# Kernel optimization log

Measured on AMD Instinct MI355X. Metric: run time of the kernel, lower is better.

## Reference

```python
import jax, jax.numpy as jnp
import numpy as np

B, T, C = 4, 2048, 1024
H = 16
D = C // H  # head_dim = 64


def setup_inputs() -> dict:
    key = jax.random.key(0)
    ks = jax.random.split(key, 9)
    s = 1.0 / np.sqrt(C)
    return {
        "x": jax.random.normal(ks[0], (B, T, C), dtype=jnp.float32),
        "wq": jax.random.uniform(ks[1], (C, C), jnp.float32, -s, s),
        "bq": jax.random.uniform(ks[2], (C,), jnp.float32, -s, s),
        "wk": jax.random.uniform(ks[3], (C, C), jnp.float32, -s, s),
        "bk": jax.random.uniform(ks[4], (C,), jnp.float32, -s, s),
        "wv": jax.random.uniform(ks[5], (C, C), jnp.float32, -s, s),
        "bv": jax.random.uniform(ks[6], (C,), jnp.float32, -s, s),
        "wo": jax.random.uniform(ks[7], (C, C), jnp.float32, -s, s),
        "bo": jax.random.uniform(ks[8], (C,), jnp.float32, -s, s),
    }


def reference(x, wq, bq, wk, bk, wv, bv, wo, bo):
    # Linear layers (torch convention: y = x @ W.T + b)
    q = x @ wq.T + bq  # [B,T,C]
    k = x @ wk.T + bk
    v = x @ wv.T + bv
    # split heads -> [B,H,T,D]
    q = q.reshape(B, T, H, D).transpose(0, 2, 1, 3)
    k = k.reshape(B, T, H, D).transpose(0, 2, 1, 3)
    v = v.reshape(B, T, H, D).transpose(0, 2, 1, 3)
    scores = jnp.einsum('bhqd,bhkd->bhqk', q, k) / jnp.sqrt(jnp.float32(D))
    causal = jnp.tril(jnp.ones((T, T), dtype=bool))  # position i attends to j<=i
    scores = jnp.where(causal, scores, -jnp.inf)
    attn = jax.nn.softmax(scores, axis=-1)
    # dropout p=0.0 (eval / identity)
    out = jnp.einsum('bhqk,bhkd->bhqd', attn, v)  # [B,H,T,D]
    out = out.transpose(0, 2, 1, 3).reshape(B, T, C)
    return out @ wo.T + bo
```

## Files before the change

### kernel.cpp

```cpp
#include <hip/hip_runtime.h>
#include <stdint.h>

#define B_DIM 4
#define T_DIM 2048
#define C_DIM 1024
#define H_DIM 16
#define D_DIM 64
#define M_DIM (B_DIM * T_DIM)
#define QK_SCALE 0.18033688011112042f

typedef float f32x4 __attribute__((ext_vector_type(4)));
typedef float f32x16 __attribute__((ext_vector_type(16)));
typedef short bf16x8 __attribute__((ext_vector_type(8)));
typedef unsigned short u16;
typedef u16 u16x8 __attribute__((ext_vector_type(8)));

static __device__ __forceinline__ u16 f2b(float f) {
  uint32_t r;
  asm("v_cvt_pk_bf16_f32 %0, %1, %1" : "=v"(r) : "v"(f));
  return (u16)r;
}
static __device__ __forceinline__ uint32_t f2b2(float a, float b) {
  uint32_t r;
  asm("v_cvt_pk_bf16_f32 %0, %1, %2" : "=v"(r) : "v"(a), "v"(b));
  return r;
}

static __device__ __forceinline__ void gl_lds16(const u16* g, u16* l) {
  __builtin_amdgcn_global_load_lds(
      (const __attribute__((address_space(1))) void*)g,
      (__attribute__((address_space(3))) void*)l, 16, 0, 0);
}

__global__ void k_cvt(const float* __restrict__ src, u16* __restrict__ dst, int n4) {
  int i = blockIdx.x * blockDim.x + threadIdx.x;
  if (i < n4) {
    float4 v = ((const float4*)src)[i];
    uint2 o;
    o.x = f2b2(v.x, v.y);
    o.y = f2b2(v.z, v.w);
    ((uint2*)dst)[i] = o;
  }
}

__global__ void k_cvtw(const float* __restrict__ s0, const float* __restrict__ s1,
                       const float* __restrict__ s2, const float* __restrict__ s3,
                       u16* __restrict__ d0, u16* __restrict__ d1,
                       u16* __restrict__ d2, u16* __restrict__ d3) {
  int i = blockIdx.x * blockDim.x + threadIdx.x;
  int seg = i >> 18;
  int j = i & ((1 << 18) - 1);
  const float* s = seg == 0 ? s0 : seg == 1 ? s1 : seg == 2 ? s2 : s3;
  u16* d = seg == 0 ? d0 : seg == 1 ? d1 : seg == 2 ? d2 : d3;
  float4 v = ((const float4*)s)[j];
  uint2 o;
  o.x = f2b2(v.x, v.y);
  o.y = f2b2(v.z, v.w);
  ((uint2*)d)[j] = o;
}

#define NT 16
__global__ __launch_bounds__(512, 2) void k_gemm_qkv(
    const u16* __restrict__ A,
    const u16* __restrict__ w0, const u16* __restrict__ w1, const u16* __restrict__ w2,
    const float* __restrict__ b0, const float* __restrict__ b1, const float* __restrict__ b2,
    u16* __restrict__ Qo, u16* __restrict__ Ko, u16* __restrict__ Vo) {
  __shared__ u16 LA[2][2][256 * 32];
  __shared__ u16 LB[2][2][256 * 32];
  const int tid = threadIdx.x;
  const int l = tid & 63;
  const int w = tid >> 6;
  const int wm = w >> 2, wn = w & 3;
  const int lrow = l & 15, lk = l >> 4;
  const int K = C_DIM;

  const int bid = blockIdx.x;
  const int swz = (bid & 7) * 48 + (bid >> 3);
  const int rowblk = swz / 12, colblk = swz % 12;
  const int seg = colblk >> 2;
  const int brow = rowblk * 256, bcol = (colblk & 3) * 256;

  const u16* Bw = seg == 0 ? w0 : seg == 1 ? w1 : w2;
  const float* bias = seg == 0 ? b0 : seg == 1 ? b1 : b2;
  u16* Out = seg == 0 ? Qo : seg == 1 ? Ko : Vo;
  const float scale = seg == 0 ? QK_SCALE : 1.f;

  const int sr0 = tid >> 2, sc0 = (tid & 3) * 8;
  const int sr1 = (tid + 512) >> 2;

#define STA(db, kh, t)                                                              \
  {                                                                                 \
    gl_lds16(A + (size_t)(brow + sr0) * K + (t) * 64 + (kh) * 32 + sc0,             \
             &LA[db][kh][sr0 * 32 + sc0]);                                          \
    gl_lds16(A + (size_t)(brow + sr1) * K + (t) * 64 + (kh) * 32 + sc0,             \
             &LA[db][kh][sr1 * 32 + sc0]);                                          \
  }
#define STB(db, kh, t)                                                              \
  {                                                                                 \
    gl_lds16(Bw + (size_t)(bcol + sr0) * K + (t) * 64 + (kh) * 32 + sc0,            \
             &LB[db][kh][sr0 * 32 + sc0]);                                          \
    gl_lds16(Bw + (size_t)(bcol + sr1) * K + (t) * 64 + (kh) * 32 + sc0,            \
             &LB[db][kh][sr1 * 32 + sc0]);                                          \
  }
#define LDA_(f, kh, db) (*(const bf16x8*)(&LA[db][kh][(wm * 128 + (f) * 16 + lrow) * 32 + lk * 8]))
#define LDB_(g, kh, db) (*(const bf16x8*)(&LB[db][kh][(wn * 64 + (g) * 16 + lrow) * 32 + lk * 8]))

  f32x4 acc[8][4];
#pragma unroll
  for (int f = 0; f < 8; ++f)
#pragma unroll
    for (int g = 0; g < 4; ++g) acc[f][g] = (f32x4){0.f, 0.f, 0.f, 0.f};

  STA(0, 0, 0); STB(0, 0, 0); STA(0, 1, 0); STB(0, 1, 0);
  asm volatile("s_waitcnt vmcnt(0)" ::: "memory");
  __syncthreads();

  for (int t = 0; t < NT; ++t) {
    const int db = t & 1, ndb = db ^ 1;
    const bool pf = (t + 1 < NT);
    bf16x8 afr[4], bfr[4];

    if (pf) STA(ndb, 0, t + 1);
#pragma unroll
    for (int g = 0; g < 4; ++g) bfr[g] = LDB_(g, 0, db);
#pragma unroll
    for (int j = 0; j < 4; ++j) afr[j] = LDA_(j, 0, db);
    __builtin_amdgcn_s_barrier();
    asm volatile("s_waitcnt lgkmcnt(0)" ::: "memory");
    __builtin_amdgcn_sched_barrier(0);
    __builtin_amdgcn_s_setprio(1);
#pragma unroll
    for (int j = 0; j < 4; ++j)
#pragma unroll
      for (int g = 0; g < 4; ++g)
        acc[j][g] = __builtin_amdgcn_mfma_f32_16x16x32_bf16(afr[j], bfr[g], acc[j][g], 0, 0, 0);
    __builtin_amdgcn_s_setprio(0);
    __builtin_amdgcn_s_barrier();

    if (pf) STB(ndb, 0, t + 1);
#pragma unroll
    for (int j = 0; j < 4; ++j) afr[j] = LDA_(4 + j, 0, db);
    __builtin_amdgcn_s_barrier();
    asm volatile("s_waitcnt lgkmcnt(0)" ::: "memory");
    __builtin_amdgcn_sched_barrier(0);
    __builtin_amdgcn_s_setprio(1);
#pragma unroll
    for (int j = 0; j < 4; ++j)
#pragma unroll
      for (int g = 0; g < 4; ++g)
        acc[4 + j][g] = __builtin_amdgcn_mfma_f32_16x16x32_bf16(afr[j], bfr[g], acc[4 + j][g], 0, 0, 0);
    __builtin_amdgcn_s_setprio(0);
    if (t == NT - 1) {
      asm volatile("s_waitcnt vmcnt(0)" ::: "memory");
    } else {
      asm volatile("s_waitcnt vmcnt(4)" ::: "memory");
    }
    __builtin_amdgcn_s_barrier();

    if (pf) STA(ndb, 1, t + 1);
#pragma unroll
    for (int g = 0; g < 4; ++g) bfr[g] = LDB_(g, 1, db);
#pragma unroll
    for (int j = 0; j < 4; ++j) afr[j] = LDA_(j, 1, db);
    __builtin_amdgcn_s_barrier();
    asm volatile("s_waitcnt lgkmcnt(0)" ::: "memory");
    __builtin_amdgcn_sched_barrier(0);
    __builtin_amdgcn_s_setprio(1);
#pragma unroll
    for (int j = 0; j < 4; ++j)
#pragma unroll
      for (int g = 0; g < 4; ++g)
        acc[j][g] = __builtin_amdgcn_mfma_f32_16x16x32_bf16(afr[j], bfr[g], acc[j][g], 0, 0, 0);
    __builtin_amdgcn_s_setprio(0);
    __builtin_amdgcn_s_barrier();

    if (pf) STB(ndb, 1, t + 1);
#pragma unroll
    for (int j = 0; j < 4; ++j) afr[j] = LDA_(4 + j, 1, db);
    __builtin_amdgcn_s_barrier();
    asm volatile("s_waitcnt lgkmcnt(0)" ::: "memory");
    __builtin_amdgcn_sched_barrier(0);
    __builtin_amdgcn_s_setprio(1);
#pragma unroll
    for (int j = 0; j < 4; ++j)
#pragma unroll
      for (int g = 0; g < 4; ++g)
        acc[4 + j][g] = __builtin_amdgcn_mfma_f32_16x16x32_bf16(afr[j], bfr[g], acc[4 + j][g], 0, 0, 0);
    __builtin_amdgcn_s_setprio(0);
    asm volatile("s_waitcnt vmcnt(4)" ::: "memory");
    __builtin_amdgcn_s_barrier();
  }

#pragma unroll
  for (int f = 0; f < 8; ++f) {
    int rg0 = brow + wm * 128 + f * 16 + lk * 4;
#pragma unroll
    for (int g = 0; g < 4; ++g) {
      int cg = bcol + wn * 64 + g * 16 + lrow;
      float bv = bias[cg];
#pragma unroll
      for (int i = 0; i < 4; ++i) {
        int rg = rg0 + i;
        float val = (acc[f][g][i] + bv) * scale;
        int bb = rg >> 11, tt = rg & (T_DIM - 1);
        int hh = cg >> 6, dd = cg & 63;
        Out[(((size_t)bb * H_DIM + hh) * T_DIM + tt) * D_DIM + dd] = f2b(val);
      }
    }
  }
#undef STA
#undef STB
#undef LDA_
#undef LDB_
}

__global__ __launch_bounds__(256) void k_gemm_proj(
    const u16* __restrict__ A, const u16* __restrict__ Bw,
    const float* __restrict__ bias, float* __restrict__ Cout) {
  __shared__ u16 As[128 * 32];
  __shared__ u16 Bs[128 * 32];
  const int tid = threadIdx.x;
  const int l = tid & 63;
  const int w = tid >> 6;
  const int wr = w >> 1, wc = w & 1;
  const int brow = blockIdx.y * 128, bcol = blockIdx.x * 128;
  const int lrow = l & 15, lk = l >> 4;
  const int K = C_DIM, N = C_DIM;

  f32x4 acc[4][4];
  for (int m = 0; m < 4; ++m)
    for (int n = 0; n < 4; ++n)
      acc[m][n] = (f32x4){0.f, 0.f, 0.f, 0.f};

  for (int kt = 0; kt < K; kt += 32) {
    __syncthreads();
    {
      int slot = tid;
      int r0 = slot >> 2, c0 = slot & 3;
      gl_lds16(A + (size_t)(brow + r0) * K + kt + c0 * 8, As + slot * 8);
      gl_lds16(Bw + (size_t)(bcol + r0) * K + kt + c0 * 8, Bs + slot * 8);
      int slot2 = slot + 256;
      int r1 = slot2 >> 2, c1 = slot2 & 3;
      gl_lds16(A + (size_t)(brow + r1) * K + kt + c1 * 8, As + slot2 * 8);
      gl_lds16(Bw + (size_t)(bcol + r1) * K + kt + c1 * 8, Bs + slot2 * 8);
    }
    asm volatile("s_waitcnt vmcnt(0)" ::: "memory");
    __syncthreads();

    bf16x8 af[4], bfr[4];
#pragma unroll
    for (int m = 0; m < 4; ++m)
      af[m] = *(const bf16x8*)(As + (wr * 64 + m * 16 + lrow) * 32 + lk * 8);
#pragma unroll
    for (int n = 0; n < 4; ++n)
      bfr[n] = *(const bf16x8*)(Bs + (wc * 64 + n * 16 + lrow) * 32 + lk * 8);
#pragma unroll
    for (int m = 0; m < 4; ++m) {
#pragma unroll
      for (int n = 0; n < 4; ++n)
        acc[m][n] = __builtin_amdgcn_mfma_f32_16x16x32_bf16(af[m], bfr[n], acc[m][n], 0, 0, 0);
    }
  }

#pragma unroll
  for (int m = 0; m < 4; ++m) {
    int rg0 = brow + wr * 64 + m * 16 + lk * 4;
#pragma unroll
    for (int n = 0; n < 4; ++n) {
      int cg = bcol + wc * 64 + n * 16 + lrow;
      float bv = bias[cg];
#pragma unroll
      for (int i = 0; i < 4; ++i)
        Cout[(size_t)(rg0 + i) * N + cg] = acc[m][n][i] + bv;
    }
  }
}

__global__ __launch_bounds__(256) void k_transpose(
    const u16* __restrict__ V, u16* __restrict__ Vt) {
  __shared__ u16 tile[64][65];
  const int tid = threadIdx.x;
  const int bh = blockIdx.y;
  const int t0 = blockIdx.x * 64;
  const size_t ibase = (size_t)bh * T_DIM * D_DIM + (size_t)t0 * D_DIM;
  const size_t obase = (size_t)bh * D_DIM * T_DIM + t0;

#pragma unroll
  for (int it = 0; it < 2; ++it) {
    int row = (tid >> 3) + it * 32;
    int blk = tid & 7;
    u16x8 v = *(const u16x8*)(V + ibase + (size_t)row * D_DIM + blk * 8);
#pragma unroll
    for (int j = 0; j < 8; ++j) tile[row][blk * 8 + j] = v[j];
  }
  __syncthreads();
#pragma unroll
  for (int it = 0; it < 2; ++it) {
    int d = (tid >> 3) + it * 32;
    int blk = tid & 7;
    u16x8 v;
#pragma unroll
    for (int j = 0; j < 8; ++j) v[j] = tile[blk * 8 + j][d];
    *(u16x8*)(Vt + obase + (size_t)d * T_DIM + blk * 8) = v;
  }
}

__global__ __launch_bounds__(256) void k_attn(
    const u16* __restrict__ Q, const u16* __restrict__ Kg,
    const u16* __restrict__ Vt, u16* __restrict__ O) {
  __shared__ u16 Ks[2][64 * 64];
  __shared__ u16 Vs[2][64 * 64];

  const int tid = threadIdx.x;
  const int l = tid & 63;
  const int w = tid >> 6;
  const int bh = blockIdx.x;
  const int qb = 15 - blockIdx.y;
  const int q0 = qb * 128;
  const int ql = l & 31;
  const int hi = l >> 5;
  const int r0 = q0 + w * 32;
  const int qg = r0 + ql;

  const size_t qkbase = (size_t)bh * T_DIM * D_DIM;
  const size_t vtbase = (size_t)bh * D_DIM * T_DIM;

  const int sr0 = tid >> 3, sc = tid & 7;
  const int sr1 = (tid + 256) >> 3;
  const int kcol0 = (sc ^ (sr0 & 7)) * 8;
  const int kcol1 = (sc ^ (sr1 & 7)) * 8;

#define STAGE(buf, kt)                                                                   \
  {                                                                                      \
    gl_lds16(Kg + qkbase + (size_t)((kt) * 64 + sr0) * D_DIM + kcol0, Ks[buf] + tid * 8);\
    gl_lds16(Vt + vtbase + (size_t)sr0 * T_DIM + (kt) * 64 + kcol0, Vs[buf] + tid * 8);  \
    gl_lds16(Kg + qkbase + (size_t)((kt) * 64 + sr1) * D_DIM + kcol1,                    \
             Ks[buf] + (tid + 256) * 8);                                                 \
    gl_lds16(Vt + vtbase + (size_t)sr1 * T_DIM + (kt) * 64 + kcol1,                      \
             Vs[buf] + (tid + 256) * 8);                                                 \
  }

  bf16x8 qf[4];
#pragma unroll
  for (int kk = 0; kk < 4; ++kk)
    qf[kk] = *(const bf16x8*)(Q + qkbase + (size_t)qg * D_DIM + kk * 16 + hi * 8);

  f32x16 oacc[2];
#pragma unroll
  for (int dt = 0; dt < 2; ++dt)
#pragma unroll
    for (int r = 0; r < 16; ++r) oacc[dt][r] = 0.f;
  float m_run = -1e30f, l_run = 0.f;

  const int tdiag = r0 >> 6;
  const int nkt = (q0 >> 6) + 2;

  STAGE(0, 0);

  for (int kt = 0; kt < nkt; ++kt) {
    const int cur = kt & 1;
    if (kt + 1 < nkt) {
      STAGE(cur ^ 1, kt + 1);
      asm volatile("s_waitcnt vmcnt(4)" ::: "memory");
    } else {
      asm volatile("s_waitcnt vmcnt(0)" ::: "memory");
    }
    __syncthreads();

    if (kt <= tdiag) {
      f32x16 s[2];
#pragma unroll
      for (int a = 0; a < 2; ++a)
#pragma unroll
        for (int r = 0; r < 16; ++r) s[a][r] = 0.f;

#pragma unroll
      for (int kk = 0; kk < 4; ++kk) {
#pragma unroll
        for (int a = 0; a < 2; ++a) {
          int row = a * 32 + ql;
          int blk = (kk * 2 + hi) ^ (row & 7);
          bf16x8 kf = *(const bf16x8*)(Ks[cur] + row * 64 + blk * 8);
          s[a] = __builtin_amdgcn_mfma_f32_32x32x16_bf16(kf, qf[kk], s[a], 0, 0, 0);
        }
      }

      if (kt == tdiag) {
#pragma unroll
        for (int a = 0; a < 2; ++a) {
#pragma unroll
          for (int r = 0; r < 16; ++r) {
            int kv = kt * 64 + a * 32 + (r & 3) + 8 * (r >> 2) + 4 * hi;
            if (kv > qg) s[a][r] = -1e30f;
          }
        }
      }

      float t[16];
#pragma unroll
      for (int r = 0; r < 16; ++r) t[r] = fmaxf(s[0][r], s[1][r]);
#pragma unroll
      for (int r = 0; r < 8; ++r) t[r] = fmaxf(t[r], t[r + 8]);
#pragma unroll
      for (int r = 0; r < 4; ++r) t[r] = fmaxf(t[r], t[r + 4]);
      float pm = fmaxf(fmaxf(t[0], t[1]), fmaxf(t[2], t[3]));
      pm = fmaxf(pm, __shfl_xor(pm, 32, 64));

      if (__any(pm > m_run + 8.f)) {
        float mn = fmaxf(m_run, pm);
        float sc_ = exp2f(m_run - mn);
        m_run = mn;
        l_run *= sc_;
#pragma unroll
        for (int dt = 0; dt < 2; ++dt)
#pragma unroll
          for (int r = 0; r < 16; ++r) oacc[dt][r] *= sc_;
      }

      float rs0 = 0.f, rs1 = 0.f, rs2 = 0.f, rs3 = 0.f;
#pragma unroll
      for (int a = 0; a < 2; ++a) {
#pragma unroll
        for (int r = 0; r < 16; ++r) {
          float p = exp2f(s[a][r] - m_run);
          s[a][r] = p;
          if ((r & 3) == 0) rs0 += p;
          else if ((r & 3) == 1) rs1 += p;
          else if ((r & 3) == 2) rs2 += p;
          else rs3 += p;
        }
      }
      float rs = (rs0 + rs1) + (rs2 + rs3);
      rs += __shfl_xor(rs, 32, 64);
      l_run += rs;

#pragma unroll
      for (int kk = 0; kk < 4; ++kk) {
        const int a = kk >> 1;
        const int base = (kk & 1) * 8;
        union { uint32_t wd[4]; bf16x8 v; } pf;
#pragma unroll
        for (int i = 0; i < 2; ++i) {
          uint32_t Aw = f2b2(s[a][base + 2 * i], s[a][base + 2 * i + 1]);
          uint32_t Bw = f2b2(s[a][base + 4 + 2 * i], s[a][base + 5 + 2 * i]);
          uint32_t As_ = (uint32_t)__shfl_xor((int)Aw, 32, 64);
          uint32_t Bs_ = (uint32_t)__shfl_xor((int)Bw, 32, 64);
          pf.wd[i] = hi ? Bs_ : Aw;
          pf.wd[2 + i] = hi ? Bw : As_;
        }
#pragma unroll
        for (int dt = 0; dt < 2; ++dt) {
          int row = dt * 32 + ql;
          int blk = (kk * 2 + hi) ^ (row & 7);
          bf16x8 vf = *(const bf16x8*)(Vs[cur] + row * 64 + blk * 8);
          oacc[dt] = __builtin_amdgcn_mfma_f32_32x32x16_bf16(vf, pf.v, oacc[dt], 0, 0, 0);
        }
      }
    }
    __syncthreads();
  }

  const int bb = bh >> 4, hh = bh & 15;
  const float inv = 1.f / l_run;
  u16* orow = O + ((size_t)bb * T_DIM + qg) * C_DIM + hh * D_DIM;
#pragma unroll
  for (int dt = 0; dt < 2; ++dt) {
#pragma unroll
    for (int g = 0; g < 4; ++g) {
      uint2 val;
      val.x = f2b2(oacc[dt][g * 4 + 0] * inv, oacc[dt][g * 4 + 1] * inv);
      val.y = f2b2(oacc[dt][g * 4 + 2] * inv, oacc[dt][g * 4 + 3] * inv);
      *(uint2*)(orow + dt * 32 + g * 8 + 4 * hi) = val;
    }
  }
}

extern "C" void kernel_launch(void* const* d_in, const int* in_sizes, int n_in,
                              void* d_out, int out_size, void* d_ws, size_t ws_size,
                              hipStream_t stream) {
  (void)in_sizes; (void)n_in; (void)out_size; (void)ws_size;
  const float* x  = (const float*)d_in[0];
  const float* wq = (const float*)d_in[1];
  const float* bq = (const float*)d_in[2];
  const float* wk = (const float*)d_in[3];
  const float* bk = (const float*)d_in[4];
  const float* wv = (const float*)d_in[5];
  const float* bv = (const float*)d_in[6];
  const float* wo = (const float*)d_in[7];
  const float* bo = (const float*)d_in[8];
  float* out = (float*)d_out;

  u16* xb  = (u16*)d_ws;
  u16* wqb = xb + (size_t)M_DIM * C_DIM;
  u16* wkb = wqb + (size_t)C_DIM * C_DIM;
  u16* wvb = wkb + (size_t)C_DIM * C_DIM;
  u16* wob = wvb + (size_t)C_DIM * C_DIM;
  u16* Qb  = wob + (size_t)C_DIM * C_DIM;
  u16* Kb  = Qb + (size_t)M_DIM * C_DIM;
  u16* Vb  = Kb + (size_t)M_DIM * C_DIM;
  u16* Vtb = Vb + (size_t)M_DIM * C_DIM;
  u16* Ob  = Vb;

  int n4x = M_DIM * C_DIM / 4;
  k_cvt<<<(n4x + 255) / 256, 256, 0, stream>>>(x, xb, n4x);
  k_cvtw<<<4096, 256, 0, stream>>>(wq, wk, wv, wo, wqb, wkb, wvb, wob);

  k_gemm_qkv<<<384, 512, 0, stream>>>(
      xb, wqb, wkb, wvb, bq, bk, bv, Qb, Kb, Vb);

  k_transpose<<<dim3(T_DIM / 64, B_DIM * H_DIM), 256, 0, stream>>>(Vb, Vtb);
  k_attn<<<dim3(B_DIM * H_DIM, 16), 256, 0, stream>>>(Qb, Kb, Vtb, Ob);
  k_gemm_proj<<<dim3(C_DIM / 128, M_DIM / 128), 256, 0, stream>>>(Ob, wob, bo, out);
}
```

Measured before the change: 224.0 us.

## Use XOR-swizzled 64-wide LDS tiles and reorder QKV GEMM prefetch stages

Switches the QKV GEMM shared-memory tiles from two 32-column halves to one 64-column row per k-tile, with an XOR swizzle of 16-byte chunks by row. This aims to cut LDS bank conflicts on the fragment reads and to make each global row load a contiguous 128 bytes. The prefetch is regrouped so B rows load first, then A rows, and the vmcnt waits are retuned to match. The waits are finer-grained, so any mistake in the vmcnt counts could cause races.

```diff
diff --git a/kernel.cpp b/kernel.cpp
--- a/kernel.cpp
+++ b/kernel.cpp
@@ -65,8 +65,8 @@
     const u16* __restrict__ w0, const u16* __restrict__ w1, const u16* __restrict__ w2,
     const float* __restrict__ b0, const float* __restrict__ b1, const float* __restrict__ b2,
     u16* __restrict__ Qo, u16* __restrict__ Ko, u16* __restrict__ Vo) {
-  __shared__ u16 LA[2][2][256 * 32];
-  __shared__ u16 LB[2][2][256 * 32];
+  __shared__ u16 LA[2][256 * 64];
+  __shared__ u16 LB[2][256 * 64];
   const int tid = threadIdx.x;
   const int l = tid & 63;
   const int w = tid >> 6;
@@ -85,25 +85,21 @@
   u16* Out = seg == 0 ? Qo : seg == 1 ? Ko : Vo;
   const float scale = seg == 0 ? QK_SCALE : 1.f;
 
-  const int sr0 = tid >> 2, sc0 = (tid & 3) * 8;
-  const int sr1 = (tid + 512) >> 2;
-
-#define STA(db, kh, t)                                                              \
-  {                                                                                 \
-    gl_lds16(A + (size_t)(brow + sr0) * K + (t) * 64 + (kh) * 32 + sc0,             \
-             &LA[db][kh][sr0 * 32 + sc0]);                                          \
-    gl_lds16(A + (size_t)(brow + sr1) * K + (t) * 64 + (kh) * 32 + sc0,             \
-             &LA[db][kh][sr1 * 32 + sc0]);                                          \
-  }
-#define STB(db, kh, t)                                                              \
-  {                                                                                 \
-    gl_lds16(Bw + (size_t)(bcol + sr0) * K + (t) * 64 + (kh) * 32 + sc0,            \
-             &LB[db][kh][sr0 * 32 + sc0]);                                          \
-    gl_lds16(Bw + (size_t)(bcol + sr1) * K + (t) * 64 + (kh) * 32 + sc0,            \
-             &LB[db][kh][sr1 * 32 + sc0]);                                          \
-  }
-#define LDA_(f, kh, db) (*(const bf16x8*)(&LA[db][kh][(wm * 128 + (f) * 16 + lrow) * 32 + lk * 8]))
-#define LDB_(g, kh, db) (*(const bf16x8*)(&LB[db][kh][(wn * 64 + (g) * 16 + lrow) * 32 + lk * 8]))
+  const int sr = tid >> 3, sc = tid & 7;
+  const int scg = (sc ^ (sr & 7)) * 8;
+
+#define STG(P, base, r0, db, t, Lx)                                               \
+  gl_lds16(P + (size_t)((base) + (r0) + sr) * K + (t) * 64 + scg,                 \
+           &Lx[db][((r0) + sr) * 64 + sc * 8])
+#define SB01(db, t) { STG(Bw, bcol, 0, db, t, LB); STG(Bw, bcol, 64, db, t, LB); }
+#define SB23(db, t) { STG(Bw, bcol, 128, db, t, LB); STG(Bw, bcol, 192, db, t, LB); }
+#define SA02(db, t) { STG(A, brow, 0, db, t, LA); STG(A, brow, 128, db, t, LA); }
+#define SA13(db, t) { STG(A, brow, 64, db, t, LA); STG(A, brow, 192, db, t, LA); }
+
+#define LDA_F(f, kk, db) (*(const bf16x8*)(&LA[db][(wm * 128 + (f) * 16 + lrow) * 64 + \
+                                                   ((((kk) * 4 + lk) ^ (lrow & 7)) * 8)]))
+#define LDB_F(g, kk, db) (*(const bf16x8*)(&LB[db][(wn * 64 + (g) * 16 + lrow) * 64 + \
+                                                   ((((kk) * 4 + lk) ^ (lrow & 7)) * 8)]))
 
   f32x4 acc[8][4];
 #pragma unroll
@@ -111,20 +107,20 @@
 #pragma unroll
     for (int g = 0; g < 4; ++g) acc[f][g] = (f32x4){0.f, 0.f, 0.f, 0.f};
 
-  STA(0, 0, 0); STB(0, 0, 0); STA(0, 1, 0); STB(0, 1, 0);
-  asm volatile("s_waitcnt vmcnt(0)" ::: "memory");
-  __syncthreads();
+  SB01(0, 0); SB23(0, 0); SA02(0, 0); SA13(0, 0);
+  asm volatile("s_waitcnt vmcnt(2)" ::: "memory");
+  __builtin_amdgcn_s_barrier();
 
   for (int t = 0; t < NT; ++t) {
     const int db = t & 1, ndb = db ^ 1;
     const bool pf = (t + 1 < NT);
     bf16x8 afr[4], bfr[4];
 
-    if (pf) STA(ndb, 0, t + 1);
-#pragma unroll
-    for (int g = 0; g < 4; ++g) bfr[g] = LDB_(g, 0, db);
-#pragma unroll
-    for (int j = 0; j < 4; ++j) afr[j] = LDA_(j, 0, db);
+    if (pf) SB01(ndb, t + 1);
+#pragma unroll
+    for (int g = 0; g < 4; ++g) bfr[g] = LDB_F(g, 0, db);
+#pragma unroll
+    for (int j = 0; j < 4; ++j) afr[j] = LDA_F(j, 0, db);
     __builtin_amdgcn_s_barrier();
     asm volatile("s_waitcnt lgkmcnt(0)" ::: "memory");
     __builtin_amdgcn_sched_barrier(0);
@@ -135,11 +131,13 @@
       for (int g = 0; g < 4; ++g)
         acc[j][g] = __builtin_amdgcn_mfma_f32_16x16x32_bf16(afr[j], bfr[g], acc[j][g], 0, 0, 0);
     __builtin_amdgcn_s_setprio(0);
-    __builtin_amdgcn_s_barrier();
-
-    if (pf) STB(ndb, 0, t + 1);
-#pragma unroll
-    for (int j = 0; j < 4; ++j) afr[j] = LDA_(4 + j, 0, db);
+    if (pf) { asm volatile("s_waitcnt vmcnt(2)" ::: "memory"); }
+    else    { asm volatile("s_waitcnt vmcnt(0)" ::: "memory"); }
+    __builtin_amdgcn_s_barrier();
+
+    if (pf) SB23(ndb, t + 1);
+#pragma unroll
+    for (int j = 0; j < 4; ++j) afr[j] = LDA_F(4 + j, 0, db);
     __builtin_amdgcn_s_barrier();
     asm volatile("s_waitcnt lgkmcnt(0)" ::: "memory");
     __builtin_amdgcn_sched_barrier(0);
@@ -150,18 +148,13 @@
       for (int g = 0; g < 4; ++g)
         acc[4 + j][g] = __builtin_amdgcn_mfma_f32_16x16x32_bf16(afr[j], bfr[g], acc[4 + j][g], 0, 0, 0);
     __builtin_amdgcn_s_setprio(0);
-    if (t == NT - 1) {
-      asm volatile("s_waitcnt vmcnt(0)" ::: "memory");
-    } else {
-      asm volatile("s_waitcnt vmcnt(4)" ::: "memory");
-    }
-    __builtin_amdgcn_s_barrier();
-
-    if (pf) STA(ndb, 1, t + 1);
-#pragma unroll
-    for (int g = 0; g < 4; ++g) bfr[g] = LDB_(g, 1, db);
-#pragma unroll
-    for (int j = 0; j < 4; ++j) afr[j] = LDA_(j, 1, db);
+    __builtin_amdgcn_s_barrier();
+
+    if (pf) SA02(ndb, t + 1);
+#pragma unroll
+    for (int g = 0; g < 4; ++g) bfr[g] = LDB_F(g, 1, db);
+#pragma unroll
+    for (int j = 0; j < 4; ++j) afr[j] = LDA_F(j, 1, db);
     __builtin_amdgcn_s_barrier();
     asm volatile("s_waitcnt lgkmcnt(0)" ::: "memory");
     __builtin_amdgcn_sched_barrier(0);
@@ -174,9 +167,9 @@
     __builtin_amdgcn_s_setprio(0);
     __builtin_amdgcn_s_barrier();
 
-    if (pf) STB(ndb, 1, t + 1);
-#pragma unroll
-    for (int j = 0; j < 4; ++j) afr[j] = LDA_(4 + j, 1, db);
+    if (pf) SA13(ndb, t + 1);
+#pragma unroll
+    for (int j = 0; j < 4; ++j) afr[j] = LDA_F(4 + j, 1, db);
     __builtin_amdgcn_s_barrier();
     asm volatile("s_waitcnt lgkmcnt(0)" ::: "memory");
     __builtin_amdgcn_sched_barrier(0);
@@ -187,7 +180,7 @@
       for (int g = 0; g < 4; ++g)
         acc[4 + j][g] = __builtin_amdgcn_mfma_f32_16x16x32_bf16(afr[j], bfr[g], acc[4 + j][g], 0, 0, 0);
     __builtin_amdgcn_s_setprio(0);
-    asm volatile("s_waitcnt vmcnt(4)" ::: "memory");
+    if (pf) { asm volatile("s_waitcnt vmcnt(2)" ::: "memory"); }
     __builtin_amdgcn_s_barrier();
   }
 
@@ -208,10 +201,13 @@
       }
     }
   }
-#undef STA
-#undef STB
-#undef LDA_
-#undef LDB_
+#undef STG
+#undef SB01
+#undef SB23
+#undef SA02
+#undef SA13
+#undef LDA_F
+#undef LDB_F
 }
 
 __global__ __launch_bounds__(256) void k_gemm_proj(
```

New measurement: 236.2 us. 5.4% more time.
